# Performance work log

Hardware: AMD Instinct MI355X
Metric: run time of the kernel (lower is better)

Reference implementation:

```python
import jax, jax.numpy as jnp
import numpy as np

M, N = 32, 32
IN_MULT, OUT_MULT = 5, 40
HQ = M * M  # 1024, hidden size of GRU_Q and GRU_Sigma; GRU_S hidden = N*N = 1024


def _l2norm(x):
    # torch F.normalize(p=2, dim=0, eps=1e-12)
    return x / jnp.maximum(jnp.linalg.norm(x), 1e-12)


def _gru(x, h, Wih, Whh, bih, bhh):
    # single-step torch nn.GRU cell, gate order r,z,n
    gi = Wih @ x + bih
    gh = Whh @ h + bhh
    Hh = h.shape[0]
    r = jax.nn.sigmoid(gi[:Hh] + gh[:Hh])
    z = jax.nn.sigmoid(gi[Hh:2 * Hh] + gh[Hh:2 * Hh])
    n = jnp.tanh(gi[2 * Hh:] + r * gh[2 * Hh:])
    return (1.0 - z) * n + z * h


def setup_inputs() -> dict:
    key = jax.random.key(0)
    ks = iter(jax.random.split(key, 48))

    def rn(shape, scale=1.0):
        return jax.random.normal(next(ks), shape, dtype=jnp.float32) * jnp.float32(scale)

    def w(o, i):
        return rn((o, i), 1.0 / np.sqrt(i))

    d_in_sigma = HQ + M * IN_MULT          # 1184
    d_in_s = N * N + 2 * N * IN_MULT       # 1344
    d_fc2_in = HQ + N * N                  # 2048
    d_fc2_hid = d_fc2_in * OUT_MULT        # 81920
    inp = dict(
        y=rn((N,)),
        m1x_posterior=rn((M, 1)), m1x_posterior_previous=rn((M, 1)),
        m1x_prior_previous=rn((M, 1)), y_previous=rn((N, 1)),
        h_Q=rn((HQ,)), h_Sigma=rn((HQ,)), h_S=rn((N * N,)),
        F=w(M, M), H=w(N, M),
        FC5_w=w(M * IN_MULT, M), FC5_b=rn((M * IN_MULT,), 0.01),
        FC6_w=w(M * IN_MULT, M), FC6_b=rn((M * IN_MULT,), 0.01),
        FC7_w=w(2 * N * IN_MULT, 2 * N), FC7_b=rn((2 * N * IN_MULT,), 0.01),
        GRUQ_Wih=w(3 * HQ, M * IN_MULT), GRUQ_Whh=w(3 * HQ, HQ),
        GRUQ_bih=rn((3 * HQ,), 0.01), GRUQ_bhh=rn((3 * HQ,), 0.01),
        GRUSig_Wih=w(3 * HQ, d_in_sigma), GRUSig_Whh=w(3 * HQ, HQ),
        GRUSig_bih=rn((3 * HQ,), 0.01), GRUSig_bhh=rn((3 * HQ,), 0.01),
        GRUS_Wih=w(3 * N * N, d_in_s), GRUS_Whh=w(3 * N * N, N * N),
        GRUS_bih=rn((3 * N * N,), 0.01), GRUS_bhh=rn((3 * N * N,), 0.01),
        FC1_w=w(N * N, HQ), FC1_b=rn((N * N,), 0.01),
        FC2_w1=w(d_fc2_hid, d_fc2_in), FC2_b1=rn((d_fc2_hid,), 0.01),
        FC2_w2=w(N * M, d_fc2_hid), FC2_b2=rn((N * M,), 0.01),
        FC3_w=w(M * M, N * N + N * M), FC3_b=rn((M * M,), 0.01),
        FC4_w=w(HQ, HQ + M * M), FC4_b=rn((HQ,), 0.01),
        fix_H_flag=1,
    )
    return inp


def _forward(y, m1x_posterior, m1x_posterior_previous, m1x_prior_previous, y_previous,
             h_Q, h_Sigma, h_S, F, H,
             FC5_w, FC5_b, FC6_w, FC6_b, FC7_w, FC7_b,
             GRUQ_Wih, GRUQ_Whh, GRUQ_bih, GRUQ_bhh,
             GRUSig_Wih, GRUSig_Whh, GRUSig_bih, GRUSig_bhh,
             GRUS_Wih, GRUS_Whh, GRUS_bih, GRUS_bhh,
             FC1_w, FC1_b, FC2_w1, FC2_b1, FC2_w2, FC2_b2,
             FC3_w, FC3_b, FC4_w, FC4_b):
    # step_prior (fix_H_flag=True path: h is linear)
    m1x_prior = F @ m1x_posterior          # [m,1]
    m1y = H @ m1x_prior                    # [n,1]
    # step_KGain_est: feature differences, L2-normalized
    obs_diff = _l2norm(y - y_previous[:, 0])
    obs_innov_diff = _l2norm(y - m1y[:, 0])
    fw_evol_diff = _l2norm(m1x_posterior[:, 0] - m1x_posterior_previous[:, 0])
    fw_update_diff = _l2norm(m1x_posterior[:, 0] - m1x_prior_previous[:, 0])
    # KGain_step (dropout layers are identity in eval)
    out_FC5 = jax.nn.relu(FC5_w @ fw_evol_diff + FC5_b)
    out_Q = _gru(out_FC5, h_Q, GRUQ_Wih, GRUQ_Whh, GRUQ_bih, GRUQ_bhh)
    out_FC6 = jax.nn.relu(FC6_w @ fw_update_diff + FC6_b)
    out_Sigma = _gru(jnp.concatenate([out_Q, out_FC6]), h_Sigma,
                     GRUSig_Wih, GRUSig_Whh, GRUSig_bih, GRUSig_bhh)
    out_FC1 = jax.nn.relu(FC1_w @ out_Sigma + FC1_b)
    out_FC7 = jax.nn.relu(FC7_w @ jnp.concatenate([obs_diff, obs_innov_diff]) + FC7_b)
    out_S = _gru(jnp.concatenate([out_FC1, out_FC7]), h_S,
                 GRUS_Wih, GRUS_Whh, GRUS_bih, GRUS_bhh)
    in_FC2 = jnp.concatenate([out_Sigma, out_S])
    out_FC2 = FC2_w2 @ jax.nn.relu(FC2_w1 @ in_FC2 + FC2_b1) + FC2_b2   # [m*n]
    out_FC3 = jax.nn.relu(FC3_w @ jnp.concatenate([out_S, out_FC2]) + FC3_b)
    out_FC4 = jax.nn.relu(FC4_w @ jnp.concatenate([out_Sigma, out_FC3]) + FC4_b)  # new h_Sigma state
    del out_FC4  # state update only; not part of returned output
    # KNet_step update
    KG = out_FC2.reshape(M, N)
    dy = y[:, None] - m1y
    m1x_posterior_new = m1x_prior + KG @ dy
    return m1x_posterior_new[:, 0]


def reference(y, m1x_posterior, m1x_posterior_previous, m1x_prior_previous, y_previous,
              h_Q, h_Sigma, h_S, F, H,
              FC5_w, FC5_b, FC6_w, FC6_b, FC7_w, FC7_b,
              GRUQ_Wih, GRUQ_Whh, GRUQ_bih, GRUQ_bhh,
              GRUSig_Wih, GRUSig_Whh, GRUSig_bih, GRUSig_bhh,
              GRUS_Wih, GRUS_Whh, GRUS_bih, GRUS_bhh,
              FC1_w, FC1_b, FC2_w1, FC2_b1, FC2_w2, FC2_b2,
              FC3_w, FC3_b, FC4_w, FC4_b, fix_H_flag):
    return _forward(y, m1x_posterior, m1x_posterior_previous, m1x_prior_previous, y_previous,
                    h_Q, h_Sigma, h_S, F, H,
                    FC5_w, FC5_b, FC6_w, FC6_b, FC7_w, FC7_b,
                    GRUQ_Wih, GRUQ_Whh, GRUQ_bih, GRUQ_bhh,
                    GRUSig_Wih, GRUSig_Whh, GRUSig_bih, GRUSig_bhh,
                    GRUS_Wih, GRUS_Whh, GRUS_bih, GRUS_bhh,
                    FC1_w, FC1_b, FC2_w1, FC2_b1, FC2_w2, FC2_b2,
                    FC3_w, FC3_b, FC4_w, FC4_b)
```

## Files before the change

### kernel.cpp

```cpp
#include <hip/hip_runtime.h>
#include <math.h>

#define DEV __device__ __forceinline__

DEV float dot4(float4 w, float4 x) {
    float s = 0.f;
    s = fmaf(w.x, x.x, s); s = fmaf(w.y, x.y, s);
    s = fmaf(w.z, x.z, s); s = fmaf(w.w, x.w, s);
    return s;
}

DEV float wave_reduce(float v) {
    for (int off = 32; off > 0; off >>= 1) v += __shfl_down(v, off);
    return v;
}
DEV float reduce32(float v) {
    for (int off = 16; off > 0; off >>= 1) v += __shfl_xor(v, off);
    return v;
}

#define WS_Q      0
#define WS_SIG    1024
#define WS_S      2048
#define WS_FC1    3072
#define WS_HID    4096
#define WS_KG     86016

DEV void gru_tail(int wid, int lane,
                  float ai0, float ai1, float ai2, float ah0, float ah1, float ah2,
                  const float* __restrict__ bih, const float* __restrict__ bhh,
                  const float* __restrict__ h, float* __restrict__ out) {
    ai0 = wave_reduce(ai0); ai1 = wave_reduce(ai1); ai2 = wave_reduce(ai2);
    ah0 = wave_reduce(ah0); ah1 = wave_reduce(ah1); ah2 = wave_reduce(ah2);
    if (lane == 0) {
        float gr = ai0 + bih[wid]        + ah0 + bhh[wid];
        float gz = ai1 + bih[wid + 1024] + ah1 + bhh[wid + 1024];
        float r = 1.f / (1.f + expf(-gr));
        float z = 1.f / (1.f + expf(-gz));
        float n = tanhf(ai2 + bih[wid + 2048] + r * (ah2 + bhh[wid + 2048]));
        out[wid] = (1.f - z) * n + z * h[wid];
    }
}

DEV void gru_hh(int wid, int lane, const float* __restrict__ Whh, const float* __restrict__ h,
                float& ah0, float& ah1, float& ah2) {
    const float4* V = (const float4*)Whh;
    const float4* v0 = V + (size_t)wid * 256;
    const float4* v1 = V + (size_t)(1024 + wid) * 256;
    const float4* v2 = V + (size_t)(2048 + wid) * 256;
    const float4* h4 = (const float4*)h;
#pragma unroll
    for (int i = 0; i < 4; ++i) {
        int k = lane + (i << 6);
        float4 hv = h4[k];
        ah0 += dot4(v0[k], hv); ah1 += dot4(v1[k], hv); ah2 += dot4(v2[k], hv);
    }
}

__global__ void k_gru_q(const float* __restrict__ post, const float* __restrict__ post_prev,
                        const float* __restrict__ fc5w, const float* __restrict__ fc5b,
                        const float* __restrict__ h,
                        const float* __restrict__ Wih, const float* __restrict__ Whh,
                        const float* __restrict__ bih, const float* __restrict__ bhh,
                        float* __restrict__ out) {
    __shared__ __align__(16) float sx[160];
    __shared__ float sd[32];
    __shared__ float sinv;
    int t = threadIdx.x;
    if (t < 32) sd[t] = post[t] - post_prev[t];
    __syncthreads();
    if (t < 64) {
        float d = (t < 32) ? sd[t] * sd[t] : 0.f;
        d = wave_reduce(d);
        if (t == 0) sinv = 1.f / fmaxf(sqrtf(d), 1e-12f);
    }
    __syncthreads();
    if (t < 160) {
        float a = 0.f;
#pragma unroll
        for (int j = 0; j < 32; ++j) a = fmaf(fc5w[t * 32 + j], sd[j], a);
        sx[t] = fmaxf(fmaf(a, sinv, fc5b[t]), 0.f);
    }
    __syncthreads();

    int wid = (blockIdx.x << 2) + (t >> 6);
    int lane = t & 63;
    const float4* W = (const float4*)Wih;
    const float4* sx4 = (const float4*)sx;
    float ai0 = 0.f, ai1 = 0.f, ai2 = 0.f, ah0 = 0.f, ah1 = 0.f, ah2 = 0.f;
    if (lane < 40) {
        float4 xv = sx4[lane];
        ai0 = dot4(W[(size_t)wid * 40 + lane], xv);
        ai1 = dot4(W[(size_t)(1024 + wid) * 40 + lane], xv);
        ai2 = dot4(W[(size_t)(2048 + wid) * 40 + lane], xv);
    }
    gru_hh(wid, lane, Whh, h, ah0, ah1, ah2);
    gru_tail(wid, lane, ai0, ai1, ai2, ah0, ah1, ah2, bih, bhh, h, out);
}

__global__ void k_gru_sigma(const float* __restrict__ xq,
                            const float* __restrict__ post, const float* __restrict__ prior_prev,
                            const float* __restrict__ fc6w, const float* __restrict__ fc6b,
                            const float* __restrict__ h,
                            const float* __restrict__ Wih, const float* __restrict__ Whh,
                            const float* __restrict__ bih, const float* __restrict__ bhh,
                            float* __restrict__ out) {
    __shared__ __align__(16) float sx[160];
    __shared__ float sd[32];
    __shared__ float sinv;
    int t = threadIdx.x;
    if (t < 32) sd[t] = post[t] - prior_prev[t];
    __syncthreads();
    if (t < 64) {
        float d = (t < 32) ? sd[t] * sd[t] : 0.f;
        d = wave_reduce(d);
        if (t == 0) sinv = 1.f / fmaxf(sqrtf(d), 1e-12f);
    }
    __syncthreads();
    if (t < 160) {
        float a = 0.f;
#pragma unroll
        for (int j = 0; j < 32; ++j) a = fmaf(fc6w[t * 32 + j], sd[j], a);
        sx[t] = fmaxf(fmaf(a, sinv, fc6b[t]), 0.f);
    }
    __syncthreads();

    int wid = (blockIdx.x << 2) + (t >> 6);
    int lane = t & 63;
    const float4* W = (const float4*)Wih;
    const float4* w0 = W + (size_t)wid * 296;
    const float4* w1 = W + (size_t)(1024 + wid) * 296;
    const float4* w2 = W + (size_t)(2048 + wid) * 296;
    const float4* q4 = (const float4*)xq;
    const float4* sx4 = (const float4*)sx;
    float ai0 = 0.f, ai1 = 0.f, ai2 = 0.f, ah0 = 0.f, ah1 = 0.f, ah2 = 0.f;
#pragma unroll
    for (int i = 0; i < 4; ++i) {
        int k = lane + (i << 6);
        float4 xv = q4[k];
        ai0 += dot4(w0[k], xv); ai1 += dot4(w1[k], xv); ai2 += dot4(w2[k], xv);
    }
    if (lane < 40) {
        int k = 256 + lane;
        float4 xv = sx4[lane];
        ai0 += dot4(w0[k], xv); ai1 += dot4(w1[k], xv); ai2 += dot4(w2[k], xv);
    }
    gru_hh(wid, lane, Whh, h, ah0, ah1, ah2);
    gru_tail(wid, lane, ai0, ai1, ai2, ah0, ah1, ah2, bih, bhh, h, out);
}

__global__ void k_gru_s(const float* __restrict__ xfc1,
                        const float* __restrict__ y, const float* __restrict__ y_prev,
                        const float* __restrict__ post,
                        const float* __restrict__ F, const float* __restrict__ Hm,
                        const float* __restrict__ fc7w, const float* __restrict__ fc7b,
                        const float* __restrict__ h,
                        const float* __restrict__ Wih, const float* __restrict__ Whh,
                        const float* __restrict__ bih, const float* __restrict__ bhh,
                        float* __restrict__ out) {
    __shared__ __align__(16) float sx[320];
    __shared__ float sprior[32];
    __shared__ float sd[2][32];
    __shared__ float sinv[2];
    int t = threadIdx.x;
    if (t < 32) {
        float p = 0.f;
#pragma unroll
        for (int j = 0; j < 32; ++j) p = fmaf(F[t * 32 + j], post[j], p);
        sprior[t] = p;
        sd[0][t] = y[t] - y_prev[t];
    }
    __syncthreads();
    if (t < 32) {
        float m = 0.f;
#pragma unroll
        for (int j = 0; j < 32; ++j) m = fmaf(Hm[t * 32 + j], sprior[j], m);
        sd[1][t] = y[t] - m;
    }
    __syncthreads();
    if (t < 64) {
        int g = t >> 5, j = t & 31;
        float d = sd[g][j];
        float s = reduce32(d * d);
        if (j == 0) sinv[g] = 1.f / fmaxf(sqrtf(s), 1e-12f);
    }
    __syncthreads();
    for (int r = t; r < 320; r += 256) {
        float a0 = 0.f, a1 = 0.f;
#pragma unroll
        for (int j = 0; j < 32; ++j) {
            a0 = fmaf(fc7w[r * 64 + j], sd[0][j], a0);
            a1 = fmaf(fc7w[r * 64 + 32 + j], sd[1][j], a1);
        }
        sx[r] = fmaxf(a0 * sinv[0] + a1 * sinv[1] + fc7b[r], 0.f);
    }
    __syncthreads();

    int wid = (blockIdx.x << 2) + (t >> 6);
    int lane = t & 63;
    const float4* W = (const float4*)Wih;
    const float4* w0 = W + (size_t)wid * 336;
    const float4* w1 = W + (size_t)(1024 + wid) * 336;
    const float4* w2 = W + (size_t)(2048 + wid) * 336;
    const float4* x4 = (const float4*)xfc1;
    const float4* sx4 = (const float4*)sx;
    float ai0 = 0.f, ai1 = 0.f, ai2 = 0.f, ah0 = 0.f, ah1 = 0.f, ah2 = 0.f;
#pragma unroll
    for (int i = 0; i < 4; ++i) {
        int k = lane + (i << 6);
        float4 xv = x4[k];
        ai0 += dot4(w0[k], xv); ai1 += dot4(w1[k], xv); ai2 += dot4(w2[k], xv);
    }
    {
        int k = 256 + lane;
        float4 xv = sx4[lane];
        ai0 += dot4(w0[k], xv); ai1 += dot4(w1[k], xv); ai2 += dot4(w2[k], xv);
    }
    if (lane < 16) {
        int k = 320 + lane;
        float4 xv = sx4[64 + lane];
        ai0 += dot4(w0[k], xv); ai1 += dot4(w1[k], xv); ai2 += dot4(w2[k], xv);
    }
    gru_hh(wid, lane, Whh, h, ah0, ah1, ah2);
    gru_tail(wid, lane, ai0, ai1, ai2, ah0, ah1, ah2, bih, bhh, h, out);
}

template <int NITER>
__global__ void k_matvec_relu(const float* __restrict__ W, const float* __restrict__ x,
                              const float* __restrict__ b, float* __restrict__ out) {
    int wid = (blockIdx.x << 2) + (threadIdx.x >> 6);
    int lane = threadIdx.x & 63;
    const float4* w4 = (const float4*)W + (size_t)wid * (NITER * 64);
    const float4* x4 = (const float4*)x;
    float a0 = 0.f, a1 = 0.f;
#pragma unroll
    for (int i = 0; i < NITER; ++i) {
        int k = lane + (i << 6);
        float v = dot4(w4[k], x4[k]);
        if (i & 1) a1 += v; else a0 += v;
    }
    float a = wave_reduce(a0 + a1);
    if (lane == 0) out[wid] = fmaxf(a + b[wid], 0.f);
}

__global__ void k_matvec_big(const float* __restrict__ W, const float* __restrict__ x,
                             const float* __restrict__ b, float* __restrict__ out) {
    int row = blockIdx.x;
    int t = threadIdx.x;
    const float4* w4 = (const float4*)W + (size_t)row * 20480;
    const float4* x4 = (const float4*)x;
    float a0 = 0.f, a1 = 0.f;
#pragma unroll 4
    for (int k = t; k < 20480; k += 512) {
        float v = dot4(w4[k], x4[k]);
        if (k & 512) a1 += v; else a0 += v;
    }
    float a = wave_reduce(a0 + a1);
    __shared__ float s[8];
    if ((t & 63) == 0) s[t >> 6] = a;
    __syncthreads();
    if (t == 0) {
        float r = b[row];
#pragma unroll
        for (int i = 0; i < 8; ++i) r += s[i];
        out[row] = r;
    }
}

__global__ void k_final(const float* __restrict__ F, const float* __restrict__ Hm,
                        const float* __restrict__ post, const float* __restrict__ y,
                        const float* __restrict__ kg, float* __restrict__ out) {
    __shared__ float sprior[32], sdy[32];
    int i = threadIdx.x;
    float p = 0.f;
#pragma unroll
    for (int j = 0; j < 32; ++j) p = fmaf(F[i * 32 + j], post[j], p);
    sprior[i] = p;
    __syncthreads();
    float m = 0.f;
#pragma unroll
    for (int j = 0; j < 32; ++j) m = fmaf(Hm[i * 32 + j], sprior[j], m);
    sdy[i] = y[i] - m;
    __syncthreads();
    float a = sprior[i];
#pragma unroll
    for (int j = 0; j < 32; ++j) a = fmaf(kg[i * 32 + j], sdy[j], a);
    out[i] = a;
}

extern "C" void kernel_launch(void* const* d_in, const int* in_sizes, int n_in,
                              void* d_out, int out_size, void* d_ws, size_t ws_size,
                              hipStream_t stream) {
    const float* y          = (const float*)d_in[0];
    const float* post       = (const float*)d_in[1];
    const float* post_prev  = (const float*)d_in[2];
    const float* prior_prev = (const float*)d_in[3];
    const float* y_prev     = (const float*)d_in[4];
    const float* h_Q        = (const float*)d_in[5];
    const float* h_Sigma    = (const float*)d_in[6];
    const float* h_S        = (const float*)d_in[7];
    const float* F          = (const float*)d_in[8];
    const float* Hm         = (const float*)d_in[9];
    const float* FC5_w      = (const float*)d_in[10];
    const float* FC5_b      = (const float*)d_in[11];
    const float* FC6_w      = (const float*)d_in[12];
    const float* FC6_b      = (const float*)d_in[13];
    const float* FC7_w      = (const float*)d_in[14];
    const float* FC7_b      = (const float*)d_in[15];
    const float* GQ_Wih     = (const float*)d_in[16];
    const float* GQ_Whh     = (const float*)d_in[17];
    const float* GQ_bih     = (const float*)d_in[18];
    const float* GQ_bhh     = (const float*)d_in[19];
    const float* GS_Wih     = (const float*)d_in[20];
    const float* GS_Whh     = (const float*)d_in[21];
    const float* GS_bih     = (const float*)d_in[22];
    const float* GS_bhh     = (const float*)d_in[23];
    const float* GU_Wih     = (const float*)d_in[24];
    const float* GU_Whh     = (const float*)d_in[25];
    const float* GU_bih     = (const float*)d_in[26];
    const float* GU_bhh     = (const float*)d_in[27];
    const float* FC1_w      = (const float*)d_in[28];
    const float* FC1_b      = (const float*)d_in[29];
    const float* FC2_w1     = (const float*)d_in[30];
    const float* FC2_b1     = (const float*)d_in[31];
    const float* FC2_w2     = (const float*)d_in[32];
    const float* FC2_b2     = (const float*)d_in[33];

    float* ws = (float*)d_ws;

    k_gru_q<<<256, 256, 0, stream>>>(post, post_prev, FC5_w, FC5_b, h_Q,
                                     GQ_Wih, GQ_Whh, GQ_bih, GQ_bhh, ws + WS_Q);
    k_gru_sigma<<<256, 256, 0, stream>>>(ws + WS_Q, post, prior_prev, FC6_w, FC6_b, h_Sigma,
                                         GS_Wih, GS_Whh, GS_bih, GS_bhh, ws + WS_SIG);
    k_matvec_relu<4><<<256, 256, 0, stream>>>(FC1_w, ws + WS_SIG, FC1_b, ws + WS_FC1);
    k_gru_s<<<256, 256, 0, stream>>>(ws + WS_FC1, y, y_prev, post, F, Hm, FC7_w, FC7_b, h_S,
                                     GU_Wih, GU_Whh, GU_bih, GU_bhh, ws + WS_S);
    k_matvec_relu<8><<<20480, 256, 0, stream>>>(FC2_w1, ws + WS_SIG, FC2_b1, ws + WS_HID);
    k_matvec_big<<<1024, 512, 0, stream>>>(FC2_w2, ws + WS_HID, FC2_b2, ws + WS_KG);
    k_final<<<1, 32, 0, stream>>>(F, Hm, post, y, ws + WS_KG, (float*)d_out);
}
```

Baseline: 205.6 us.

## Overlap FC2 first-layer halves with GRU stages and use nontemporal weight loads

Restructures the launch sequence so the FC2_w1 matvec is split by input half. The half that depends on the Sigma output runs inside the same kernels as FC1 and GRU_S, and the S-dependent half plus bias and ReLU runs afterwards. The FC5/FC6/FC7 preprocessing is merged into one stage, and each GRU row now gets a full 256-thread block instead of one wavefront. All weight streams are read with nontemporal loads so they do not pollute the cache. This trades an extra read-modify-write of the hidden vector and a more complex workspace layout for better overlap and more parallelism in the small, latency-bound GRU stages.

```diff
diff --git a/kernel.cpp b/kernel.cpp
--- a/kernel.cpp
+++ b/kernel.cpp
@@ -3,7 +3,11 @@
 
 #define DEV __device__ __forceinline__
 
-DEV float dot4(float4 w, float4 x) {
+typedef float f4 __attribute__((ext_vector_type(4)));
+
+DEV f4 ntl(const f4* p) { return __builtin_nontemporal_load(p); }
+
+DEV float dot4(f4 w, f4 x) {
     float s = 0.f;
     s = fmaf(w.x, x.x, s); s = fmaf(w.y, x.y, s);
     s = fmaf(w.z, x.z, s); s = fmaf(w.w, x.w, s);
@@ -19,240 +23,248 @@
     return v;
 }
 
-#define WS_Q      0
-#define WS_SIG    1024
-#define WS_S      2048
-#define WS_FC1    3072
-#define WS_HID    4096
-#define WS_KG     86016
-
-DEV void gru_tail(int wid, int lane,
-                  float ai0, float ai1, float ai2, float ah0, float ah1, float ah2,
-                  const float* __restrict__ bih, const float* __restrict__ bhh,
-                  const float* __restrict__ h, float* __restrict__ out) {
+#define WS_Q     0
+#define WS_FC6   1024
+#define WS_SIG   1184
+#define WS_FC1   2208
+#define WS_FC7   3232
+#define WS_S     3552
+#define WS_HID   4576
+#define WS_KG    86496
+
+template <int K4X>
+DEV void gru_row(int row, int t, const float* __restrict__ x,
+                 const float* __restrict__ h,
+                 const float* __restrict__ Wih, const float* __restrict__ Whh,
+                 const float* __restrict__ bih, const float* __restrict__ bhh,
+                 float* __restrict__ out) {
+    const f4* x4 = (const f4*)x;
+    const f4* w0 = (const f4*)Wih + (size_t)row * K4X;
+    const f4* w1 = (const f4*)Wih + (size_t)(1024 + row) * K4X;
+    const f4* w2 = (const f4*)Wih + (size_t)(2048 + row) * K4X;
+    float ai0 = 0.f, ai1 = 0.f, ai2 = 0.f;
+    if (K4X >= 256 || t < K4X) {
+        f4 xv = x4[t];
+        ai0 = dot4(ntl(w0 + t), xv);
+        ai1 = dot4(ntl(w1 + t), xv);
+        ai2 = dot4(ntl(w2 + t), xv);
+    }
+    if (K4X > 256) {
+        if (t < K4X - 256) {
+            int k = 256 + t;
+            f4 xv = x4[k];
+            ai0 += dot4(ntl(w0 + k), xv);
+            ai1 += dot4(ntl(w1 + k), xv);
+            ai2 += dot4(ntl(w2 + k), xv);
+        }
+    }
+    const f4* v0 = (const f4*)Whh + (size_t)row * 256;
+    const f4* v1 = (const f4*)Whh + (size_t)(1024 + row) * 256;
+    const f4* v2 = (const f4*)Whh + (size_t)(2048 + row) * 256;
+    f4 hv = ((const f4*)h)[t];
+    float ah0 = dot4(ntl(v0 + t), hv);
+    float ah1 = dot4(ntl(v1 + t), hv);
+    float ah2 = dot4(ntl(v2 + t), hv);
     ai0 = wave_reduce(ai0); ai1 = wave_reduce(ai1); ai2 = wave_reduce(ai2);
     ah0 = wave_reduce(ah0); ah1 = wave_reduce(ah1); ah2 = wave_reduce(ah2);
+    __shared__ float red[4][6];
+    int w = t >> 6, lane = t & 63;
     if (lane == 0) {
-        float gr = ai0 + bih[wid]        + ah0 + bhh[wid];
-        float gz = ai1 + bih[wid + 1024] + ah1 + bhh[wid + 1024];
+        red[w][0] = ai0; red[w][1] = ai1; red[w][2] = ai2;
+        red[w][3] = ah0; red[w][4] = ah1; red[w][5] = ah2;
+    }
+    __syncthreads();
+    if (t == 0) {
+        float AI0 = red[0][0] + red[1][0] + red[2][0] + red[3][0];
+        float AI1 = red[0][1] + red[1][1] + red[2][1] + red[3][1];
+        float AI2 = red[0][2] + red[1][2] + red[2][2] + red[3][2];
+        float AH0 = red[0][3] + red[1][3] + red[2][3] + red[3][3];
+        float AH1 = red[0][4] + red[1][4] + red[2][4] + red[3][4];
+        float AH2 = red[0][5] + red[1][5] + red[2][5] + red[3][5];
+        float gr = AI0 + bih[row]        + AH0 + bhh[row];
+        float gz = AI1 + bih[row + 1024] + AH1 + bhh[row + 1024];
         float r = 1.f / (1.f + expf(-gr));
         float z = 1.f / (1.f + expf(-gz));
-        float n = tanhf(ai2 + bih[wid + 2048] + r * (ah2 + bhh[wid + 2048]));
-        out[wid] = (1.f - z) * n + z * h[wid];
-    }
-}
-
-DEV void gru_hh(int wid, int lane, const float* __restrict__ Whh, const float* __restrict__ h,
-                float& ah0, float& ah1, float& ah2) {
-    const float4* V = (const float4*)Whh;
-    const float4* v0 = V + (size_t)wid * 256;
-    const float4* v1 = V + (size_t)(1024 + wid) * 256;
-    const float4* v2 = V + (size_t)(2048 + wid) * 256;
-    const float4* h4 = (const float4*)h;
+        float n = tanhf(AI2 + bih[row + 2048] + r * (AH2 + bhh[row + 2048]));
+        out[row] = (1.f - z) * n + z * h[row];
+    }
+}
+
+__global__ __launch_bounds__(256) void k_stage1(
+        const float* __restrict__ y, const float* __restrict__ y_prev,
+        const float* __restrict__ post, const float* __restrict__ post_prev,
+        const float* __restrict__ prior_prev,
+        const float* __restrict__ F, const float* __restrict__ Hm,
+        const float* __restrict__ fc5w, const float* __restrict__ fc5b,
+        const float* __restrict__ fc6w, const float* __restrict__ fc6b,
+        const float* __restrict__ fc7w, const float* __restrict__ fc7b,
+        const float* __restrict__ h_Q,
+        const float* __restrict__ Wih, const float* __restrict__ Whh,
+        const float* __restrict__ bih, const float* __restrict__ bhh,
+        float* __restrict__ ws) {
+    int t = threadIdx.x;
+    if (blockIdx.x < 1024) {
+        __shared__ __align__(16) float sx[160];
+        __shared__ float sd[32];
+        __shared__ float sinv;
+        if (t < 32) sd[t] = post[t] - post_prev[t];
+        __syncthreads();
+        if (t < 64) {
+            float d = (t < 32) ? sd[t] * sd[t] : 0.f;
+            d = wave_reduce(d);
+            if (t == 0) sinv = 1.f / fmaxf(sqrtf(d), 1e-12f);
+        }
+        __syncthreads();
+        if (t < 160) {
+            float a = 0.f;
+#pragma unroll
+            for (int j = 0; j < 32; ++j) a = fmaf(fc5w[t * 32 + j], sd[j], a);
+            sx[t] = fmaxf(fmaf(a, sinv, fc5b[t]), 0.f);
+        }
+        __syncthreads();
+        gru_row<40>(blockIdx.x, t, sx, h_Q, Wih, Whh, bih, bhh, ws + WS_Q);
+    } else if (blockIdx.x == 1024) {
+        __shared__ float sd[32];
+        __shared__ float sinv;
+        if (t < 32) sd[t] = post[t] - prior_prev[t];
+        __syncthreads();
+        if (t < 64) {
+            float d = (t < 32) ? sd[t] * sd[t] : 0.f;
+            d = wave_reduce(d);
+            if (t == 0) sinv = 1.f / fmaxf(sqrtf(d), 1e-12f);
+        }
+        __syncthreads();
+        if (t < 160) {
+            float a = 0.f;
+#pragma unroll
+            for (int j = 0; j < 32; ++j) a = fmaf(fc6w[t * 32 + j], sd[j], a);
+            ws[WS_FC6 + t] = fmaxf(fmaf(a, sinv, fc6b[t]), 0.f);
+        }
+    } else {
+        __shared__ float sp[32], sd0[32], sd1[32];
+        __shared__ float sinv0, sinv1;
+        if (t < 32) {
+            float p = 0.f;
+#pragma unroll
+            for (int j = 0; j < 32; ++j) p = fmaf(F[t * 32 + j], post[j], p);
+            sp[t] = p;
+            sd0[t] = y[t] - y_prev[t];
+        }
+        __syncthreads();
+        if (t < 32) {
+            float m = 0.f;
+#pragma unroll
+            for (int j = 0; j < 32; ++j) m = fmaf(Hm[t * 32 + j], sp[j], m);
+            sd1[t] = y[t] - m;
+        }
+        __syncthreads();
+        if (t < 64) {
+            int g = t >> 5, j = t & 31;
+            float d = g ? sd1[j] : sd0[j];
+            float s = reduce32(d * d);
+            if (j == 0) {
+                float inv = 1.f / fmaxf(sqrtf(s), 1e-12f);
+                if (g) sinv1 = inv; else sinv0 = inv;
+            }
+        }
+        __syncthreads();
+        for (int r = t; r < 320; r += 256) {
+            float a0 = 0.f, a1 = 0.f;
+#pragma unroll
+            for (int j = 0; j < 32; ++j) {
+                a0 = fmaf(fc7w[r * 64 + j], sd0[j], a0);
+                a1 = fmaf(fc7w[r * 64 + 32 + j], sd1[j], a1);
+            }
+            ws[WS_FC7 + r] = fmaxf(a0 * sinv0 + a1 * sinv1 + fc7b[r], 0.f);
+        }
+    }
+}
+
+__global__ __launch_bounds__(256) void k_stage2(
+        const float* __restrict__ h, const float* __restrict__ Wih,
+        const float* __restrict__ Whh, const float* __restrict__ bih,
+        const float* __restrict__ bhh, float* __restrict__ ws) {
+    gru_row<296>(blockIdx.x, threadIdx.x, ws + WS_Q, h, Wih, Whh, bih, bhh, ws + WS_SIG);
+}
+
+DEV void w1a_wave(int wid, int t, const float* __restrict__ W1, float* __restrict__ ws) {
+    int lane = t & 63;
+    const f4* w4 = (const f4*)W1 + (size_t)wid * 512;
+    const f4* x4 = (const f4*)(ws + WS_SIG);
+    float a0 = 0.f, a1 = 0.f;
 #pragma unroll
     for (int i = 0; i < 4; ++i) {
         int k = lane + (i << 6);
-        float4 hv = h4[k];
-        ah0 += dot4(v0[k], hv); ah1 += dot4(v1[k], hv); ah2 += dot4(v2[k], hv);
-    }
-}
-
-__global__ void k_gru_q(const float* __restrict__ post, const float* __restrict__ post_prev,
-                        const float* __restrict__ fc5w, const float* __restrict__ fc5b,
-                        const float* __restrict__ h,
-                        const float* __restrict__ Wih, const float* __restrict__ Whh,
-                        const float* __restrict__ bih, const float* __restrict__ bhh,
-                        float* __restrict__ out) {
-    __shared__ __align__(16) float sx[160];
-    __shared__ float sd[32];
-    __shared__ float sinv;
+        float v = dot4(ntl(w4 + k), x4[k]);
+        if (i & 1) a1 += v; else a0 += v;
+    }
+    float a = wave_reduce(a0 + a1);
+    if (lane == 0) ws[WS_HID + wid] = a;
+}
+
+__global__ __launch_bounds__(256) void k_stage3(
+        const float* __restrict__ W1, const float* __restrict__ fc1w,
+        const float* __restrict__ fc1b, float* __restrict__ ws) {
     int t = threadIdx.x;
-    if (t < 32) sd[t] = post[t] - post_prev[t];
-    __syncthreads();
-    if (t < 64) {
-        float d = (t < 32) ? sd[t] * sd[t] : 0.f;
-        d = wave_reduce(d);
-        if (t == 0) sinv = 1.f / fmaxf(sqrtf(d), 1e-12f);
-    }
-    __syncthreads();
-    if (t < 160) {
-        float a = 0.f;
-#pragma unroll
-        for (int j = 0; j < 32; ++j) a = fmaf(fc5w[t * 32 + j], sd[j], a);
-        sx[t] = fmaxf(fmaf(a, sinv, fc5b[t]), 0.f);
-    }
-    __syncthreads();
-
-    int wid = (blockIdx.x << 2) + (t >> 6);
-    int lane = t & 63;
-    const float4* W = (const float4*)Wih;
-    const float4* sx4 = (const float4*)sx;
-    float ai0 = 0.f, ai1 = 0.f, ai2 = 0.f, ah0 = 0.f, ah1 = 0.f, ah2 = 0.f;
-    if (lane < 40) {
-        float4 xv = sx4[lane];
-        ai0 = dot4(W[(size_t)wid * 40 + lane], xv);
-        ai1 = dot4(W[(size_t)(1024 + wid) * 40 + lane], xv);
-        ai2 = dot4(W[(size_t)(2048 + wid) * 40 + lane], xv);
-    }
-    gru_hh(wid, lane, Whh, h, ah0, ah1, ah2);
-    gru_tail(wid, lane, ai0, ai1, ai2, ah0, ah1, ah2, bih, bhh, h, out);
-}
-
-__global__ void k_gru_sigma(const float* __restrict__ xq,
-                            const float* __restrict__ post, const float* __restrict__ prior_prev,
-                            const float* __restrict__ fc6w, const float* __restrict__ fc6b,
-                            const float* __restrict__ h,
-                            const float* __restrict__ Wih, const float* __restrict__ Whh,
-                            const float* __restrict__ bih, const float* __restrict__ bhh,
-                            float* __restrict__ out) {
-    __shared__ __align__(16) float sx[160];
-    __shared__ float sd[32];
-    __shared__ float sinv;
+    if (blockIdx.x < 1024) {
+        int row = blockIdx.x;
+        const f4* w4 = (const f4*)fc1w + (size_t)row * 256;
+        const f4* x4 = (const f4*)(ws + WS_SIG);
+        float a = dot4(ntl(w4 + t), x4[t]);
+        a = wave_reduce(a);
+        __shared__ float s[4];
+        if ((t & 63) == 0) s[t >> 6] = a;
+        __syncthreads();
+        if (t == 0) ws[WS_FC1 + row] = fmaxf(s[0] + s[1] + s[2] + s[3] + fc1b[row], 0.f);
+    } else {
+        int wid = ((blockIdx.x - 1024) << 2) + (t >> 6);
+        w1a_wave(wid, t, W1, ws);
+    }
+}
+
+__global__ __launch_bounds__(256) void k_stage4(
+        const float* __restrict__ W1, const float* __restrict__ h,
+        const float* __restrict__ Wih, const float* __restrict__ Whh,
+        const float* __restrict__ bih, const float* __restrict__ bhh,
+        float* __restrict__ ws) {
     int t = threadIdx.x;
-    if (t < 32) sd[t] = post[t] - prior_prev[t];
-    __syncthreads();
-    if (t < 64) {
-        float d = (t < 32) ? sd[t] * sd[t] : 0.f;
-        d = wave_reduce(d);
-        if (t == 0) sinv = 1.f / fmaxf(sqrtf(d), 1e-12f);
-    }
-    __syncthreads();
-    if (t < 160) {
-        float a = 0.f;
-#pragma unroll
-        for (int j = 0; j < 32; ++j) a = fmaf(fc6w[t * 32 + j], sd[j], a);
-        sx[t] = fmaxf(fmaf(a, sinv, fc6b[t]), 0.f);
-    }
-    __syncthreads();
-
-    int wid = (blockIdx.x << 2) + (t >> 6);
-    int lane = t & 63;
-    const float4* W = (const float4*)Wih;
-    const float4* w0 = W + (size_t)wid * 296;
-    const float4* w1 = W + (size_t)(1024 + wid) * 296;
-    const float4* w2 = W + (size_t)(2048 + wid) * 296;
-    const float4* q4 = (const float4*)xq;
-    const float4* sx4 = (const float4*)sx;
-    float ai0 = 0.f, ai1 = 0.f, ai2 = 0.f, ah0 = 0.f, ah1 = 0.f, ah2 = 0.f;
+    if (blockIdx.x < 1024) {
+        gru_row<336>(blockIdx.x, t, ws + WS_FC1, h, Wih, Whh, bih, bhh, ws + WS_S);
+    } else {
+        int wid = 40960 + ((blockIdx.x - 1024) << 2) + (t >> 6);
+        w1a_wave(wid, t, W1, ws);
+    }
+}
+
+__global__ __launch_bounds__(256) void k_w1b(
+        const float* __restrict__ W1, const float* __restrict__ b1,
+        float* __restrict__ ws) {
+    int wid = (blockIdx.x << 2) + (threadIdx.x >> 6);
+    int lane = threadIdx.x & 63;
+    const f4* w4 = (const f4*)W1 + (size_t)wid * 512 + 256;
+    const f4* x4 = (const f4*)(ws + WS_S);
+    float a0 = 0.f, a1 = 0.f;
 #pragma unroll
     for (int i = 0; i < 4; ++i) {
         int k = lane + (i << 6);
-        float4 xv = q4[k];
-        ai0 += dot4(w0[k], xv); ai1 += dot4(w1[k], xv); ai2 += dot4(w2[k], xv);
-    }
-    if (lane < 40) {
-        int k = 256 + lane;
-        float4 xv = sx4[lane];
-        ai0 += dot4(w0[k], xv); ai1 += dot4(w1[k], xv); ai2 += dot4(w2[k], xv);
-    }
-    gru_hh(wid, lane, Whh, h, ah0, ah1, ah2);
-    gru_tail(wid, lane, ai0, ai1, ai2, ah0, ah1, ah2, bih, bhh, h, out);
-}
-
-__global__ void k_gru_s(const float* __restrict__ xfc1,
-                        const float* __restrict__ y, const float* __restrict__ y_prev,
-                        const float* __restrict__ post,
-                        const float* __restrict__ F, const float* __restrict__ Hm,
-                        const float* __restrict__ fc7w, const float* __restrict__ fc7b,
-                        const float* __restrict__ h,
-                        const float* __restrict__ Wih, const float* __restrict__ Whh,
-                        const float* __restrict__ bih, const float* __restrict__ bhh,
-                        float* __restrict__ out) {
-    __shared__ __align__(16) float sx[320];
-    __shared__ float sprior[32];
-    __shared__ float sd[2][32];
-    __shared__ float sinv[2];
-    int t = threadIdx.x;
-    if (t < 32) {
-        float p = 0.f;
-#pragma unroll
-        for (int j = 0; j < 32; ++j) p = fmaf(F[t * 32 + j], post[j], p);
-        sprior[t] = p;
-        sd[0][t] = y[t] - y_prev[t];
-    }
-    __syncthreads();
-    if (t < 32) {
-        float m = 0.f;
-#pragma unroll
-        for (int j = 0; j < 32; ++j) m = fmaf(Hm[t * 32 + j], sprior[j], m);
-        sd[1][t] = y[t] - m;
-    }
-    __syncthreads();
-    if (t < 64) {
-        int g = t >> 5, j = t & 31;
-        float d = sd[g][j];
-        float s = reduce32(d * d);
-        if (j == 0) sinv[g] = 1.f / fmaxf(sqrtf(s), 1e-12f);
-    }
-    __syncthreads();
-    for (int r = t; r < 320; r += 256) {
-        float a0 = 0.f, a1 = 0.f;
-#pragma unroll
-        for (int j = 0; j < 32; ++j) {
-            a0 = fmaf(fc7w[r * 64 + j], sd[0][j], a0);
-            a1 = fmaf(fc7w[r * 64 + 32 + j], sd[1][j], a1);
-        }
-        sx[r] = fmaxf(a0 * sinv[0] + a1 * sinv[1] + fc7b[r], 0.f);
-    }
-    __syncthreads();
-
-    int wid = (blockIdx.x << 2) + (t >> 6);
-    int lane = t & 63;
-    const float4* W = (const float4*)Wih;
-    const float4* w0 = W + (size_t)wid * 336;
-    const float4* w1 = W + (size_t)(1024 + wid) * 336;
-    const float4* w2 = W + (size_t)(2048 + wid) * 336;
-    const float4* x4 = (const float4*)xfc1;
-    const float4* sx4 = (const float4*)sx;
-    float ai0 = 0.f, ai1 = 0.f, ai2 = 0.f, ah0 = 0.f, ah1 = 0.f, ah2 = 0.f;
-#pragma unroll
-    for (int i = 0; i < 4; ++i) {
-        int k = lane + (i << 6);
-        float4 xv = x4[k];
-        ai0 += dot4(w0[k], xv); ai1 += dot4(w1[k], xv); ai2 += dot4(w2[k], xv);
-    }
-    {
-        int k = 256 + lane;
-        float4 xv = sx4[lane];
-        ai0 += dot4(w0[k], xv); ai1 += dot4(w1[k], xv); ai2 += dot4(w2[k], xv);
-    }
-    if (lane < 16) {
-        int k = 320 + lane;
-        float4 xv = sx4[64 + lane];
-        ai0 += dot4(w0[k], xv); ai1 += dot4(w1[k], xv); ai2 += dot4(w2[k], xv);
-    }
-    gru_hh(wid, lane, Whh, h, ah0, ah1, ah2);
-    gru_tail(wid, lane, ai0, ai1, ai2, ah0, ah1, ah2, bih, bhh, h, out);
-}
-
-template <int NITER>
-__global__ void k_matvec_relu(const float* __restrict__ W, const float* __restrict__ x,
-                              const float* __restrict__ b, float* __restrict__ out) {
-    int wid = (blockIdx.x << 2) + (threadIdx.x >> 6);
-    int lane = threadIdx.x & 63;
-    const float4* w4 = (const float4*)W + (size_t)wid * (NITER * 64);
-    const float4* x4 = (const float4*)x;
-    float a0 = 0.f, a1 = 0.f;
-#pragma unroll
-    for (int i = 0; i < NITER; ++i) {
-        int k = lane + (i << 6);
-        float v = dot4(w4[k], x4[k]);
+        float v = dot4(ntl(w4 + k), x4[k]);
         if (i & 1) a1 += v; else a0 += v;
     }
     float a = wave_reduce(a0 + a1);
-    if (lane == 0) out[wid] = fmaxf(a + b[wid], 0.f);
-}
-
-__global__ void k_matvec_big(const float* __restrict__ W, const float* __restrict__ x,
-                             const float* __restrict__ b, float* __restrict__ out) {
+    if (lane == 0) ws[WS_HID + wid] = fmaxf(ws[WS_HID + wid] + a + b1[wid], 0.f);
+}
+
+__global__ __launch_bounds__(512) void k_w2(
+        const float* __restrict__ W2, const float* __restrict__ b2,
+        float* __restrict__ ws) {
     int row = blockIdx.x;
     int t = threadIdx.x;
-    const float4* w4 = (const float4*)W + (size_t)row * 20480;
-    const float4* x4 = (const float4*)x;
+    const f4* w4 = (const f4*)W2 + (size_t)row * 20480;
+    const f4* x4 = (const f4*)(ws + WS_HID);
     float a0 = 0.f, a1 = 0.f;
 #pragma unroll 4
     for (int k = t; k < 20480; k += 512) {
-        float v = dot4(w4[k], x4[k]);
+        float v = dot4(ntl(w4 + k), x4[k]);
         if (k & 512) a1 += v; else a0 += v;
     }
     float a = wave_reduce(a0 + a1);
@@ -260,10 +272,10 @@
     if ((t & 63) == 0) s[t >> 6] = a;
     __syncthreads();
     if (t == 0) {
-        float r = b[row];
+        float r = b2[row];
 #pragma unroll
         for (int i = 0; i < 8; ++i) r += s[i];
-        out[row] = r;
+        ws[WS_KG + row] = r;
     }
 }
 
@@ -328,14 +340,13 @@
 
     float* ws = (float*)d_ws;
 
-    k_gru_q<<<256, 256, 0, stream>>>(post, post_prev, FC5_w, FC5_b, h_Q,
-                                     GQ_Wih, GQ_Whh, GQ_bih, GQ_bhh, ws + WS_Q);
-    k_gru_sigma<<<256, 256, 0, stream>>>(ws + WS_Q, post, prior_prev, FC6_w, FC6_b, h_Sigma,
-                                         GS_Wih, GS_Whh, GS_bih, GS_bhh, ws + WS_SIG);
-    k_matvec_relu<4><<<256, 256, 0, stream>>>(FC1_w, ws + WS_SIG, FC1_b, ws + WS_FC1);
-    k_gru_s<<<256, 256, 0, stream>>>(ws + WS_FC1, y, y_prev, post, F, Hm, FC7_w, FC7_b, h_S,
-                                     GU_Wih, GU_Whh, GU_bih, GU_bhh, ws + WS_S);
-    k_matvec_relu<8><<<20480, 256, 0, stream>>>(FC2_w1, ws + WS_SIG, FC2_b1, ws + WS_HID);
-    k_matvec_big<<<1024, 512, 0, stream>>>(FC2_w2, ws + WS_HID, FC2_b2, ws + WS_KG);
+    k_stage1<<<1026, 256, 0, stream>>>(y, y_prev, post, post_prev, prior_prev, F, Hm,
+                                       FC5_w, FC5_b, FC6_w, FC6_b, FC7_w, FC7_b,
+                                       h_Q, GQ_Wih, GQ_Whh, GQ_bih, GQ_bhh, ws);
+    k_stage2<<<1024, 256, 0, stream>>>(h_Sigma, GS_Wih, GS_Whh, GS_bih, GS_bhh, ws);
+    k_stage3<<<11264, 256, 0, stream>>>(FC2_w1, FC1_w, FC1_b, ws);
+    k_stage4<<<11264, 256, 0, stream>>>(FC2_w1, h_S, GU_Wih, GU_Whh, GU_bih, GU_bhh, ws);
+    k_w1b<<<20480, 256, 0, stream>>>(FC2_w1, FC2_b1, ws);
+    k_w2<<<1024, 512, 0, stream>>>(FC2_w2, FC2_b2, ws);
     k_final<<<1, 32, 0, stream>>>(F, Hm, post, y, ws + WS_KG, (float*)d_out);
 }
```

Result: faster. 181.9 us (-11.5%).
